# Kernel optimization log

Hardware: AMD Instinct MI355X
Metric: run time of the kernel (lower is better)

Reference implementation:

```python
import jax, jax.numpy as jnp
import numpy as np
from jax import lax

B, T, D, H = 32, 1024, 512, 256  # batch, max_len, feature dim, per-direction hidden
NL = 2  # num LSTM layers


def _lstm_dir(x, tmask, Wih, Whh, b):
    # x: [B,T,D_in], tmask: [B,T] valid-step mask. PyTorch gate order: i,f,g,o.
    Bn = x.shape[0]
    h0 = jnp.zeros((Bn, H), x.dtype)

    def step(carry, inp):
        h, c = carry
        x_t, m_t = inp
        gates = x_t @ Wih.T + h @ Whh.T + b
        i, f, g, o = jnp.split(gates, 4, axis=-1)
        c_new = jax.nn.sigmoid(f) * c + jax.nn.sigmoid(i) * jnp.tanh(g)
        h_new = jax.nn.sigmoid(o) * jnp.tanh(c_new)
        m = m_t[:, None]
        # packed-sequence semantics: state frozen and output zero past seq length
        return (jnp.where(m, h_new, h), jnp.where(m, c_new, c)), jnp.where(m, h_new, 0.0)

    _, ys = lax.scan(step, (h0, h0), (x.transpose(1, 0, 2), tmask.T))
    return ys.transpose(1, 0, 2)


def _rev_valid(x, lens):
    # reverse each sequence within its own valid length (packed reverse direction)
    t = jnp.arange(x.shape[1])[None, :]
    idx = jnp.where(t < lens[:, None], lens[:, None] - 1 - t, t)
    return jnp.take_along_axis(x, idx[:, :, None], axis=1)


def _bilstm(x, lens, Wih, Whh, bih, bhh):
    tmask = jnp.arange(x.shape[1])[None, :] < lens[:, None]
    h = x
    for layer in range(NL):  # small fixed structural loop (dropout inactive in eval)
        fwd = _lstm_dir(h, tmask, Wih[layer, 0], Whh[layer, 0], bih[layer, 0] + bhh[layer, 0])
        bwd = _rev_valid(_lstm_dir(_rev_valid(h, lens), tmask, Wih[layer, 1], Whh[layer, 1], bih[layer, 1] + bhh[layer, 1]), lens)
        h = jnp.concatenate([fwd, bwd], axis=-1)
    return h


def setup_inputs() -> dict:
    key = jax.random.key(0)
    ks = jax.random.split(key, 12)
    s = 1.0 / np.sqrt(H)  # PyTorch LSTM init bound
    u = lambda k, shp: jax.random.uniform(k, shp, jnp.float32, -s, s)
    input_tensor = jax.random.normal(ks[0], (B, T, D), jnp.float32)
    # enforce_sorted=True -> descending lengths
    input_len = jnp.sort(jax.random.randint(ks[1], (B,), T // 2, T + 1))[::-1].astype(jnp.int64)
    mask = jnp.ones((B, T), dtype=bool)
    return {
        "input_tensor": input_tensor,
        "input_len": input_len,
        "k": 2,
        "mask": mask,
        "lstm_Wih": u(ks[2], (NL, 2, 4 * H, D)),
        "lstm_Whh": u(ks[3], (NL, 2, 4 * H, H)),
        "lstm_bih": u(ks[4], (NL, 2, 4 * H)),
        "lstm_bhh": u(ks[5], (NL, 2, 4 * H)),
        "lin_W": u(ks[6], (1, D)),
        "lin_b": u(ks[7], (1,)),
        "ln_gamma": jnp.ones((D,), jnp.float32),
        "ln_beta": jnp.zeros((D,), jnp.float32),
    }


def reference(input_tensor, input_len, k, mask, lstm_Wih, lstm_Whh, lstm_bih, lstm_bhh, lin_W, lin_b, ln_gamma, ln_beta):
    lstm_o = _bilstm(input_tensor, input_len, lstm_Wih, lstm_Whh, lstm_bih, lstm_bhh)  # [B,T,512]
    logits = (lstm_o @ lin_W.T + lin_b)[..., 0]  # [B,T]
    probs = jax.nn.softmax(logits, axis=-1)
    _, indices = lax.top_k(-probs, k)  # k lowest-probability frames per batch
    mu = jnp.mean(lstm_o, axis=-1, keepdims=True)
    var = jnp.mean(jnp.square(lstm_o - mu), axis=-1, keepdims=True)
    ln_out = (lstm_o - mu) / jnp.sqrt(var + 1e-5) * ln_gamma + ln_beta
    # vectorized scatter replacing the per-batch python loop
    sgn_mask = mask.at[jnp.arange(mask.shape[0])[:, None], indices].set(False)
    return ln_out, sgn_mask
```

## Files before the change

### kernel.cpp

```cpp
#include <hip/hip_runtime.h>
#include <stdint.h>


typedef _Float16 half8 __attribute__((ext_vector_type(8)));
typedef _Float16 half4v __attribute__((ext_vector_type(4)));
typedef float f32x4 __attribute__((ext_vector_type(4)));
typedef unsigned int uint4v __attribute__((ext_vector_type(4)));
typedef unsigned int uint2v __attribute__((ext_vector_type(2)));

#define N_X    (32768*512)
#define N_WIH  (2*2*1024*512)
#define N_WHH  (2*2*1024*256)
#define N_BIAS (2*2*1024)

__global__ __launch_bounds__(256) void k_prep(
    const float* __restrict__ x, const float* __restrict__ wih,
    const float* __restrict__ whh, const float* __restrict__ bih,
    const float* __restrict__ bhh, _Float16* __restrict__ xf,
    _Float16* __restrict__ wihf, _Float16* __restrict__ whhf,
    float* __restrict__ bias)
{
  const int total = N_X + N_WIH + N_WHH + N_BIAS;
  for (int i = blockIdx.x*256 + threadIdx.x; i < total; i += gridDim.x*256) {
    if (i < N_X) xf[i] = (_Float16)x[i];
    else if (i < N_X + N_WIH) wihf[i - N_X] = (_Float16)wih[i - N_X];
    else if (i < N_X + N_WIH + N_WHH) whhf[i - N_X - N_WIH] = (_Float16)whh[i - N_X - N_WIH];
    else { int j = i - N_X - N_WIH - N_WHH; bias[j] = bih[j] + bhh[j]; }
  }
}

__global__ __launch_bounds__(256) void k_gemm(
    const _Float16* __restrict__ A, const _Float16* __restrict__ Bw,
    const float* __restrict__ bias, _Float16* __restrict__ C)
{
  __shared__ __align__(16) _Float16 As[128*32];
  __shared__ __align__(16) _Float16 Bs[128*32];
  const int ti = blockIdx.x, tj = blockIdx.y;
  const int tid = threadIdx.x, l = tid & 63, w = tid >> 6;
  const int wm = w >> 1, wn = w & 1;
  f32x4 acc[4][4] = {};
  for (int kk = 0; kk < 512; kk += 32) {
    __syncthreads();
#pragma unroll
    for (int p = 0; p < 2; ++p) {
      int idx = p*256 + tid;
      int r = idx >> 2, c = (idx & 3) * 8;
      *(uint4v*)(As + idx*8) = *(const uint4v*)(A + (size_t)(ti*128 + r)*512 + kk + c);
      *(uint4v*)(Bs + idx*8) = *(const uint4v*)(Bw + (size_t)(tj*128 + r)*512 + kk + c);
    }
    __syncthreads();
    half8 af[4], bfr[4];
#pragma unroll
    for (int m = 0; m < 4; ++m)
      af[m] = *(const half8*)(As + (wm*64 + m*16 + (l&15))*32 + (l>>4)*8);
#pragma unroll
    for (int n = 0; n < 4; ++n)
      bfr[n] = *(const half8*)(Bs + (wn*64 + n*16 + (l&15))*32 + (l>>4)*8);
#pragma unroll
    for (int m = 0; m < 4; ++m)
#pragma unroll
      for (int n = 0; n < 4; ++n)
        acc[m][n] = __builtin_amdgcn_mfma_f32_16x16x32_f16(af[m], bfr[n], acc[m][n], 0, 0, 0);
  }
  const int colb = tj*128 + wn*64 + (l & 15);
  const int rowb = ti*128 + wm*64 + ((l >> 4) << 2);
#pragma unroll
  for (int n = 0; n < 4; ++n) {
    int cg = colb + n*16;
    float bv = bias[cg];
    int dirb = cg >> 10, g = (cg >> 8) & 3, col = cg & 255;
    size_t nc = (size_t)dirb*1024 + col*4 + g;
#pragma unroll
    for (int m = 0; m < 4; ++m)
#pragma unroll
      for (int j = 0; j < 4; ++j)
        C[(size_t)(rowb + m*16 + j)*2048 + nc] = (_Float16)(acc[m][n][j] + bv);
  }
}

__device__ __forceinline__ float sigf(float x) {
  return __fdividef(1.f, 1.f + __expf(-x));
}
__device__ __forceinline__ float tanh_fast(float x) {
  float e = __expf(-2.f * fabsf(x));
  float r = __fdividef(1.f - e, 1.f + e);
  return x < 0.f ? -r : r;
}

__global__ __launch_bounds__(512, 2) void k_rec(
    const _Float16* __restrict__ Gx,
    const _Float16* __restrict__ Whh,
    const long long* __restrict__ lens_raw,
    _Float16* __restrict__ Hout,
    _Float16* __restrict__ pub,
    unsigned int* __restrict__ flags)
{
  const int bid = blockIdx.x;
  const int sub = bid & 7;
  if (sub >= 2) return;
  const int dir = sub, q = bid >> 3;
  const int wid = dir*4 + q;
  const int tid = threadIdx.x, w8 = tid >> 6, l = tid & 63;
  const int lq = l >> 4;
  const int rh = w8 >> 2;
  const int colq = w8 & 3;
  const int ncl = colq*16 + (l & 15);

  __shared__ __align__(16) _Float16 hbuf[2*32*256];
  __shared__ int s_fast;
  for (int i = tid; i < 2*32*256; i += 512) hbuf[i] = (_Float16)0.f;

  int xcc;
  asm volatile("s_getreg_b32 %0, hwreg(HW_REG_XCC_ID)" : "=s"(xcc));
  unsigned int* xcdbuf = flags + 1024;
  if (tid == 0) {
    __hip_atomic_store(&xcdbuf[wid], (unsigned)(xcc + 1),
                       __ATOMIC_RELEASE, __HIP_MEMORY_SCOPE_AGENT);
    unsigned vv[4];
    for (int i = 0; i < 4; ++i) {
      unsigned u;
      do {
        u = __hip_atomic_load(&xcdbuf[dir*4 + i],
                              __ATOMIC_ACQUIRE, __HIP_MEMORY_SCOPE_AGENT);
      } while (u == 0);
      vv[i] = u;
    }
    s_fast = (vv[0]==vv[1] && vv[1]==vv[2] && vv[2]==vv[3]) ? 1 : 0;
  }

  half8 Bf[4][8];
#pragma unroll
  for (int g = 0; g < 4; ++g)
#pragma unroll
    for (int kt = 0; kt < 8; ++kt)
      Bf[g][kt] = *(const half8*)(Whh + ((size_t)dir*1024 + g*256 + q*64 + ncl)*256 + kt*32 + lq*8);

  int mylen[4];
  {
    bool ok64 = true;
    long long tmp[4];
#pragma unroll
    for (int j = 0; j < 4; ++j) {
      long long vv = lens_raw[rh*16 + lq*4 + j];
      tmp[j] = vv;
      ok64 = ok64 && (vv >= 1 && vv <= 1024);
    }
    const int* l32 = (const int*)lens_raw;
#pragma unroll
    for (int j = 0; j < 4; ++j)
      mylen[j] = ok64 ? (int)tmp[j] : l32[rh*16 + lq*4 + j];
  }

  float cst[4] = {};
  half4v gpf[4];

#pragma unroll
  for (int j = 0; j < 4; ++j) {
    int grow = rh*16 + lq*4 + j;
    int t = dir == 0 ? 0 : mylen[j] - 1;
    gpf[j] = *(const half4v*)(Gx + ((size_t)grow*1024 + t)*2048 + dir*1024 + ((q*64 + ncl) << 2));
  }

  const int str = tid >> 4;
  const int cb4 = (tid & 15) * 4;
  const int wsrc = ((str >> 4) << 2) + ((tid & 15) >> 2);
  int qp_[3];
#pragma unroll
  for (int i = 0; i < 3; ++i) qp_[i] = i + (i >= q ? 1 : 0);
  volatile const unsigned* vf0 = &flags[((dir*4 + qp_[0])*8 + wsrc)*16];
  volatile const unsigned* vf1 = &flags[((dir*4 + qp_[1])*8 + wsrc)*16];
  volatile const unsigned* vf2 = &flags[((dir*4 + qp_[2])*8 + wsrc)*16];

  __syncthreads();
  const bool FAST = (s_fast != 0);

  for (int s = 0; s < 1024; ++s) {
    const int p = s & 1;
    const int pr_base = p * 16384;
    const int pw_base = (p ^ 1) * 16384;

    f32x4 acc[4];
#pragma unroll
    for (int g = 0; g < 4; ++g)
#pragma unroll
      for (int j = 0; j < 4; ++j) acc[g][j] = (float)gpf[j][g];

#pragma unroll
    for (int j = 0; j < 4; ++j) {
      int grow = rh*16 + lq*4 + j;
      int t = dir == 0 ? s + 1 : mylen[j] - 2 - s;
      t = t < 0 ? 0 : (t > 1023 ? 1023 : t);
      gpf[j] = *(const half4v*)(Gx + ((size_t)grow*1024 + t)*2048 + dir*1024 + ((q*64 + ncl) << 2));
    }

#pragma unroll
    for (int kt = 0; kt < 8; ++kt) {
      int row = rh*16 + (l & 15);
      int byte = pr_base + ((row*512 + kt*64 + lq*16) ^ ((row & 7) << 4));
      half8 a = *(const half8*)((const char*)hbuf + byte);
#pragma unroll
      for (int g = 0; g < 4; ++g)
        acc[g] = __builtin_amdgcn_mfma_f32_16x16x32_f16(a, Bf[g][kt], acc[g], 0, 0, 0);
    }

    _Float16* mypub = pub + ((size_t)p*8 + wid)*2048;
#pragma unroll
    for (int j = 0; j < 4; ++j) {
      float gi = sigf(acc[0][j]);
      float gf = sigf(acc[1][j]);
      float gg = tanh_fast(acc[2][j]);
      float go = sigf(acc[3][j]);
      float cn = gf*cst[j] + gi*gg;
      cst[j] = cn;
      float hn = go * tanh_fast(cn);
      _Float16 h16 = (_Float16)hn;
      int r = rh*16 + lq*4 + j;
      int colg = q*64 + ncl;
      int byte = pw_base + ((r*512 + colg*2) ^ ((r & 7) << 4));
      *(_Float16*)((char*)hbuf + byte) = h16;
      mypub[r*64 + ncl] = h16;
      if (s < mylen[j]) {
        int t = dir == 0 ? s : mylen[j] - 1 - s;
        Hout[((size_t)r*1024 + t)*512 + dir*256 + colg] = h16;
      }
    }

    if (FAST) {
      asm volatile("s_waitcnt vmcnt(0)" ::: "memory");
      if (l == 0) flags[(wid*8 + w8)*16] = (unsigned)(s + 1);
      asm volatile("" ::: "memory");
      unsigned f0, f1, f2;
      int guard = 0;
      do {
        f0 = *vf0; f1 = *vf1; f2 = *vf2;
        if (++guard > (1 << 22)) break;
      } while (f0 <= (unsigned)s || f1 <= (unsigned)s || f2 <= (unsigned)s);
    } else {
      __threadfence();
      if (l == 0)
        __hip_atomic_store(&flags[(wid*8 + w8)*16], (unsigned)(s + 1),
                           __ATOMIC_RELAXED, __HIP_MEMORY_SCOPE_AGENT);
      unsigned f0, f1, f2;
      int guard = 0;
      do {
        f0 = __hip_atomic_load((const unsigned*)vf0, __ATOMIC_RELAXED, __HIP_MEMORY_SCOPE_AGENT);
        f1 = __hip_atomic_load((const unsigned*)vf1, __ATOMIC_RELAXED, __HIP_MEMORY_SCOPE_AGENT);
        f2 = __hip_atomic_load((const unsigned*)vf2, __ATOMIC_RELAXED, __HIP_MEMORY_SCOPE_AGENT);
        if (++guard > (1 << 22)) break;
      } while (f0 <= (unsigned)s || f1 <= (unsigned)s || f2 <= (unsigned)s);
      __threadfence();
    }

#pragma unroll
    for (int i = 0; i < 3; ++i) {
      int qp = qp_[i];
      const volatile uint2v* vp =
          (const volatile uint2v*)(pub + ((size_t)p*8 + dir*4 + qp)*2048 + str*64 + cb4);
      uint2v d = *vp;
      int byte = pw_base + ((str*512 + (qp*64 + cb4)*2) ^ ((str & 7) << 4));
      *(uint2v*)((char*)hbuf + byte) = d;
    }
    __syncthreads();
  }
}

__global__ __launch_bounds__(256) void k_head1(
    const _Float16* __restrict__ H, const float* __restrict__ linW,
    const float* __restrict__ linb, const float* __restrict__ gamma,
    const float* __restrict__ beta, float* __restrict__ lnout,
    float* __restrict__ logits)
{
  const int r = blockIdx.x*4 + (threadIdx.x >> 6);
  const int l = threadIdx.x & 63;
  half8 hv = *(const half8*)(H + (size_t)r*512 + l*8);
  f32x4 wa = *(const f32x4*)(linW + l*8);
  f32x4 wb = *(const f32x4*)(linW + l*8 + 4);
  float x[8], wv[8];
#pragma unroll
  for (int j = 0; j < 8; ++j) x[j] = (float)hv[j];
#pragma unroll
  for (int j = 0; j < 4; ++j) { wv[j] = wa[j]; wv[j+4] = wb[j]; }
  float s1 = 0.f, s2 = 0.f, sd = 0.f;
#pragma unroll
  for (int j = 0; j < 8; ++j) { s1 += x[j]; s2 += x[j]*x[j]; sd += x[j]*wv[j]; }
#pragma unroll
  for (int off = 32; off >= 1; off >>= 1) {
    s1 += __shfl_xor(s1, off);
    s2 += __shfl_xor(s2, off);
    sd += __shfl_xor(sd, off);
  }
  float mu = s1 * (1.f/512.f);
  float var = s2 * (1.f/512.f) - mu*mu;
  var = var < 0.f ? 0.f : var;
  float rstd = rsqrtf(var + 1e-5f);
  f32x4 ga = *(const f32x4*)(gamma + l*8);
  f32x4 gb = *(const f32x4*)(gamma + l*8 + 4);
  f32x4 ba = *(const f32x4*)(beta + l*8);
  f32x4 bb = *(const f32x4*)(beta + l*8 + 4);
  f32x4 oa, ob;
#pragma unroll
  for (int j = 0; j < 4; ++j) {
    oa[j] = (x[j]   - mu)*rstd*ga[j] + ba[j];
    ob[j] = (x[j+4] - mu)*rstd*gb[j] + bb[j];
  }
  *(f32x4*)(lnout + (size_t)r*512 + l*8) = oa;
  *(f32x4*)(lnout + (size_t)r*512 + l*8 + 4) = ob;
  if (l == 0) logits[r] = sd + linb[0];
}

__global__ __launch_bounds__(256) void k_head2(
    const float* __restrict__ logits, const void* __restrict__ maskraw,
    float* __restrict__ outmask)
{
  __shared__ float swv[4];
  __shared__ int   swi[4];
  __shared__ int   sidx[2];
  const int b = blockIdx.x, tid = threadIdx.x;
  const float* lg = logits + b*1024;
  float lv[4]; int ltt[4];
#pragma unroll
  for (int i = 0; i < 4; ++i) { ltt[i] = tid + i*256; lv[i] = lg[ltt[i]]; }
  int excl = -1;
  for (int pass = 0; pass < 2; ++pass) {
    float bv = 3.0e38f; int bi = 1 << 30;
#pragma unroll
    for (int i = 0; i < 4; ++i)
      if (ltt[i] != excl && (lv[i] < bv || (lv[i] == bv && ltt[i] < bi))) { bv = lv[i]; bi = ltt[i]; }
#pragma unroll
    for (int off = 32; off >= 1; off >>= 1) {
      float ov = __shfl_xor(bv, off); int oi = __shfl_xor(bi, off);
      if (ov < bv || (ov == bv && oi < bi)) { bv = ov; bi = oi; }
    }
    if ((tid & 63) == 0) { swv[tid >> 6] = bv; swi[tid >> 6] = bi; }
    __syncthreads();
    if (tid == 0) {
      float fv = swv[0]; int fi = swi[0];
      for (int u = 1; u < 4; ++u)
        if (swv[u] < fv || (swv[u] == fv && swi[u] < fi)) { fv = swv[u]; fi = swi[u]; }
      sidx[pass] = fi;
    }
    __syncthreads();
    excl = sidx[0];
    __syncthreads();
  }
  const int i1 = sidx[0], i2 = sidx[1];
  const unsigned char* mb = (const unsigned char*)maskraw;
  const bool mode8 = mb[1] != 0;
#pragma unroll
  for (int i = 0; i < 4; ++i) {
    int t = tid + i*256;
    bool mv = mode8 ? (mb[b*1024 + t] != 0)
                    : (((const int*)maskraw)[b*1024 + t] != 0);
    outmask[b*1024 + t] = (mv && t != i1 && t != i2) ? 1.f : 0.f;
  }
}

extern "C" void kernel_launch(void* const* d_in, const int* in_sizes, int n_in,
                              void* d_out, int out_size, void* d_ws, size_t ws_size,
                              hipStream_t stream) {
  const float* x      = (const float*)d_in[0];
  const long long* ln = (const long long*)d_in[1];
  const void* maskraw = d_in[3];
  const float* wih    = (const float*)d_in[4];
  const float* whh    = (const float*)d_in[5];
  const float* bih    = (const float*)d_in[6];
  const float* bhh    = (const float*)d_in[7];
  const float* linW   = (const float*)d_in[8];
  const float* linb   = (const float*)d_in[9];
  const float* gamma  = (const float*)d_in[10];
  const float* beta   = (const float*)d_in[11];
  float* out = (float*)d_out;

  char* ws = (char*)d_ws;
  _Float16* Xf   = (_Float16*)(ws + 0);
  _Float16* Hc0  = (_Float16*)(ws + 33554432);
  _Float16* Hc1  = (_Float16*)(ws + 67108864);
  _Float16* Gx   = (_Float16*)(ws + 100663296);
  _Float16* Wihf = (_Float16*)(ws + 234881024);
  _Float16* Whhf = (_Float16*)(ws + 239075328);
  float*    bias = (float*)   (ws + 241172480);
  _Float16* pub0 = (_Float16*)(ws + 241188864);
  _Float16* pub1 = (_Float16*)(ws + 241254400);
  unsigned int* flg = (unsigned int*)(ws + 241319936);
  float*  logits = (float*)   (ws + 241336320);
  if (ws_size < 241500000) return;

  hipMemsetAsync(Hc0, 0, 33554432, stream);
  hipMemsetAsync(Hc1, 0, 33554432, stream);
  hipMemsetAsync(flg, 0, 16384, stream);

  k_prep<<<4096, 256, 0, stream>>>(x, wih, whh, bih, bhh, Xf, Wihf, Whhf, bias);

  k_gemm<<<dim3(256, 16), 256, 0, stream>>>(Xf, Wihf, bias, Gx);
  k_rec<<<32, 512, 0, stream>>>(Gx, Whhf, ln, Hc0, pub0, flg);
  k_gemm<<<dim3(256, 16), 256, 0, stream>>>(Hc0, Wihf + 2*1024*512, bias + 2048, Gx);
  k_rec<<<32, 512, 0, stream>>>(Gx, Whhf + 2*1024*256, ln, Hc1, pub1, flg + 2048);

  k_head1<<<8192, 256, 0, stream>>>(Hc1, linW, linb, gamma, beta, out, logits);
  k_head2<<<32, 256, 0, stream>>>(logits, maskraw, out + 16777216);
}
```

Measured before the change: 6.428 ms.

## Pack peer step flags into one vector poll and widen h exchange copies

Step-completion flags from the four column-quarter blocks of a row group now sit contiguously, so each thread polls all peers with a single 16-byte volatile load and takes the minimum, instead of three separate scalar polls on padded lines. The copy of peer hidden-state slices from the global publish buffer into LDS now uses 16-byte vectors, with threads split so that some copy two chunks. The goal is to cut per-timestep synchronisation latency and load count in the serial recurrence. In exchange, four flags now share one cache line, which can add write contention, and the flag indexing and copy mapping must stay consistent with the writer layout.

```diff
diff --git a/kernel.cpp b/kernel.cpp
--- a/kernel.cpp
+++ b/kernel.cpp
@@ -161,15 +161,21 @@
     gpf[j] = *(const half4v*)(Gx + ((size_t)grow*1024 + t)*2048 + dir*1024 + ((q*64 + ncl) << 2));
   }
 
-  const int str = tid >> 4;
-  const int cb4 = (tid & 15) * 4;
-  const int wsrc = ((str >> 4) << 2) + ((tid & 15) >> 2);
   int qp_[3];
 #pragma unroll
   for (int i = 0; i < 3; ++i) qp_[i] = i + (i >= q ? 1 : 0);
-  volatile const unsigned* vf0 = &flags[((dir*4 + qp_[0])*8 + wsrc)*16];
-  volatile const unsigned* vf1 = &flags[((dir*4 + qp_[1])*8 + wsrc)*16];
-  volatile const unsigned* vf2 = &flags[((dir*4 + qp_[2])*8 + wsrc)*16];
+  const int c1  = tid;
+  const int i1  = c1 >> 8;
+  const int rr  = (c1 & 255) >> 3;
+  const int cg  = c1 & 7;
+  const int w8p = ((c1 & 255) >> 7)*4 + (cg >> 1);
+  const int qpa = qp_[i1];
+  const int qpb = qp_[2];
+  const bool two = (tid < 256);
+  const volatile uint4v* fquad =
+      (const volatile uint4v*)(flags + dir*128 + w8p*16);
+  const int dsta = ((rr*512 + (qpa*64 + cg*8)*2) ^ ((rr & 7) << 4));
+  const int dstb = ((rr*512 + (qpb*64 + cg*8)*2) ^ ((rr & 7) << 4));
 
   __syncthreads();
   const bool FAST = (s_fast != 0);
@@ -227,38 +233,52 @@
 
     if (FAST) {
       asm volatile("s_waitcnt vmcnt(0)" ::: "memory");
-      if (l == 0) flags[(wid*8 + w8)*16] = (unsigned)(s + 1);
+      if (l == 0) flags[dir*128 + w8*16 + q] = (unsigned)(s + 1);
       asm volatile("" ::: "memory");
-      unsigned f0, f1, f2;
       int guard = 0;
+      unsigned mn;
       do {
-        f0 = *vf0; f1 = *vf1; f2 = *vf2;
+        uint4v f = *fquad;
+        unsigned a = f[0] < f[1] ? f[0] : f[1];
+        unsigned b = f[2] < f[3] ? f[2] : f[3];
+        mn = a < b ? a : b;
         if (++guard > (1 << 22)) break;
-      } while (f0 <= (unsigned)s || f1 <= (unsigned)s || f2 <= (unsigned)s);
+      } while (mn <= (unsigned)s);
+      {
+        const volatile uint4v* spa =
+            (const volatile uint4v*)(pub + ((size_t)p*8 + dir*4 + qpa)*2048 + rr*64 + cg*8);
+        uint4v da = *spa;
+        *(uint4v*)((char*)hbuf + pw_base + dsta) = da;
+        if (two) {
+          const volatile uint4v* spb =
+              (const volatile uint4v*)(pub + ((size_t)p*8 + dir*4 + qpb)*2048 + rr*64 + cg*8);
+          uint4v db = *spb;
+          *(uint4v*)((char*)hbuf + pw_base + dstb) = db;
+        }
+      }
     } else {
       __threadfence();
       if (l == 0)
-        __hip_atomic_store(&flags[(wid*8 + w8)*16], (unsigned)(s + 1),
+        __hip_atomic_store(&flags[dir*128 + w8*16 + q], (unsigned)(s + 1),
                            __ATOMIC_RELAXED, __HIP_MEMORY_SCOPE_AGENT);
       unsigned f0, f1, f2;
       int guard = 0;
+      const unsigned* fb = flags + dir*128 + w8p*16;
       do {
-        f0 = __hip_atomic_load((const unsigned*)vf0, __ATOMIC_RELAXED, __HIP_MEMORY_SCOPE_AGENT);
-        f1 = __hip_atomic_load((const unsigned*)vf1, __ATOMIC_RELAXED, __HIP_MEMORY_SCOPE_AGENT);
-        f2 = __hip_atomic_load((const unsigned*)vf2, __ATOMIC_RELAXED, __HIP_MEMORY_SCOPE_AGENT);
+        f0 = __hip_atomic_load(fb + qp_[0], __ATOMIC_RELAXED, __HIP_MEMORY_SCOPE_AGENT);
+        f1 = __hip_atomic_load(fb + qp_[1], __ATOMIC_RELAXED, __HIP_MEMORY_SCOPE_AGENT);
+        f2 = __hip_atomic_load(fb + qp_[2], __ATOMIC_RELAXED, __HIP_MEMORY_SCOPE_AGENT);
         if (++guard > (1 << 22)) break;
       } while (f0 <= (unsigned)s || f1 <= (unsigned)s || f2 <= (unsigned)s);
       __threadfence();
-    }
-
-#pragma unroll
-    for (int i = 0; i < 3; ++i) {
-      int qp = qp_[i];
-      const volatile uint2v* vp =
-          (const volatile uint2v*)(pub + ((size_t)p*8 + dir*4 + qp)*2048 + str*64 + cb4);
-      uint2v d = *vp;
-      int byte = pw_base + ((str*512 + (qp*64 + cb4)*2) ^ ((str & 7) << 4));
-      *(uint2v*)((char*)hbuf + byte) = d;
+      {
+        uint4v da = *(const uint4v*)(pub + ((size_t)p*8 + dir*4 + qpa)*2048 + rr*64 + cg*8);
+        *(uint4v*)((char*)hbuf + pw_base + dsta) = da;
+        if (two) {
+          uint4v db = *(const uint4v*)(pub + ((size_t)p*8 + dir*4 + qpb)*2048 + rr*64 + cg*8);
+          *(uint4v*)((char*)hbuf + pw_base + dstb) = db;
+        }
+      }
     }
     __syncthreads();
   }
```

Result: faster. 5.826 ms (-9.4%).
